# Optimization experiments

Measured on AMD Instinct MI355X. Metric: run time of the kernel, lower is better.

The kernel has to match this reference:

```python
import jax, jax.numpy as jnp
import numpy as np

IN_DIM = 256
OUT_DIM = 64   # per-head dim
NUM_HEADS = 8
B = 8
N = 1024


def setup_inputs() -> dict:
    key = jax.random.key(0)
    k_adj, k_h, kq, kk, kv, kbq, kbk, kbv = jax.random.split(key, 8)
    adj_matrix = jax.random.randint(k_adj, (N, N), 0, 2, dtype=jnp.int32)
    h = jax.random.normal(k_h, (B, N, IN_DIM), dtype=jnp.float32)
    s = 1.0 / np.sqrt(IN_DIM)
    Wq = jax.random.normal(kq, (IN_DIM, OUT_DIM * NUM_HEADS), dtype=jnp.float32) * s
    Wk = jax.random.normal(kk, (IN_DIM, OUT_DIM * NUM_HEADS), dtype=jnp.float32) * s
    Wv = jax.random.normal(kv, (IN_DIM, OUT_DIM * NUM_HEADS), dtype=jnp.float32) * s
    bq = jax.random.normal(kbq, (OUT_DIM * NUM_HEADS,), dtype=jnp.float32) * 0.01
    bk = jax.random.normal(kbk, (OUT_DIM * NUM_HEADS,), dtype=jnp.float32) * 0.01
    bv = jax.random.normal(kbv, (OUT_DIM * NUM_HEADS,), dtype=jnp.float32) * 0.01
    return {"adj_matrix": adj_matrix, "h": h, "Wq": Wq, "bq": bq,
            "Wk": Wk, "bk": bk, "Wv": Wv, "bv": bv}


def reference(adj_matrix, h, Wq, bq, Wk, bk, Wv, bv):
    B_, N_, _ = h.shape
    H, D = NUM_HEADS, OUT_DIM
    Qh = (h @ Wq + bq).reshape(B_, N_, H, D)
    Kh = (h @ Wk + bk).reshape(B_, N_, H, D)
    Vh = (h @ Wv + bv).reshape(B_, N_, H, D)
    scores = jnp.einsum('bnhd,bmhd->bhnm', Qh, Kh) / jnp.sqrt(jnp.float32(D))
    # adjacency mask broadcast over batch and heads (neigh_attention=True)
    scores = jnp.where(adj_matrix[None, None, :, :] == 0, -jnp.inf, scores)
    attn = jax.nn.softmax(scores, axis=-1)
    out = jnp.einsum('bhnm,bmhd->bnhd', attn, Vh)
    return out.reshape(B_, N_, H * D)
```

## Files before the change

kernel.cpp:

```cpp
#include <hip/hip_runtime.h>
#include <hip/hip_bf16.h>
#include <math.h>

#define IN_DIM 256
#define HD     512
#define NHEADS 8
#define DH     64
#define NSEQ   1024
#define BATCH  8

#define QSCALE 0.18033688011112042f

typedef unsigned short u16;
typedef unsigned int   u32;
typedef short bf16x8 __attribute__((ext_vector_type(8)));
typedef float f32x4  __attribute__((ext_vector_type(4)));
typedef float f32x16 __attribute__((ext_vector_type(16)));
typedef unsigned int u32x2 __attribute__((ext_vector_type(2)));

#if __has_builtin(__builtin_amdgcn_exp2f)
#define EXP2(x) __builtin_amdgcn_exp2f(x)
#else
#define EXP2(x) __expf(0.69314718056f * (x))
#endif

static __device__ __forceinline__ u16 f2bf(float x) {
    u32 u = __builtin_bit_cast(u32, x);
    u += 0x7FFFu + ((u >> 16) & 1u);
    return (u16)(u >> 16);
}
static __device__ __forceinline__ u32 pk(u16 a, u16 b) {
    return (u32)a | ((u32)b << 16);
}
static __device__ __forceinline__ u32 cvtpk(float a, float b) {
    __hip_bfloat162 t = __float22bfloat162_rn(make_float2(a, b));
    u32 r; __builtin_memcpy(&r, &t, 4);
    return r;
}
static __device__ __forceinline__ f32x16 maskinit(uint4 a, uint4 b) {
    f32x16 c;
    u32 ws[8] = {a.x, a.y, a.z, a.w, b.x, b.y, b.z, b.w};
#pragma unroll
    for (int i = 0; i < 8; ++i) {
        c[2 * i]     = __builtin_bit_cast(float, ws[i] << 16);
        c[2 * i + 1] = __builtin_bit_cast(float, ws[i] & 0xFFFF0000u);
    }
    return c;
}

static __device__ __forceinline__ void pswap(u32 &a, u32 &b) {
#if __has_builtin(__builtin_amdgcn_permlane32_swap)
    u32x2 r = __builtin_amdgcn_permlane32_swap(a, b, false, false);
    a = r.x; b = r.y;
#else
    const bool hi = (threadIdx.x & 32) != 0;
    u32 as = (u32)__shfl_xor((int)a, 32, 64);
    u32 bs = (u32)__shfl_xor((int)b, 32, 64);
    u32 na = hi ? bs : a;
    u32 nb = hi ? b  : as;
    a = na; b = nb;
#endif
}

#define MFMA32(a, b, c) __builtin_amdgcn_mfma_f32_32x32x16_bf16(a, b, c, 0, 0, 0)

#define GLOAD16(G, L)                                                          \
    __builtin_amdgcn_global_load_lds(                                          \
        (const __attribute__((address_space(1))) unsigned int*)(const void*)(G),\
        (__attribute__((address_space(3))) unsigned int*)(void*)(L), 16, 0, 0)

static __device__ __forceinline__ float sm_pack_half(const f32x16 st, bf16x8* pb) {
    float p[16];
#pragma unroll
    for (int r = 0; r < 16; ++r) p[r] = EXP2(st[r]);
    float t = (((p[0] + p[1]) + (p[2] + p[3])) + ((p[4] + p[5]) + (p[6] + p[7])))
            + (((p[8] + p[9]) + (p[10] + p[11])) + ((p[12] + p[13]) + (p[14] + p[15])));
    uint4 w0, w1;
    w0.x = cvtpk(p[0], p[1]);   w0.y = cvtpk(p[2], p[3]);
    w0.z = cvtpk(p[4], p[5]);   w0.w = cvtpk(p[6], p[7]);
    w1.x = cvtpk(p[8], p[9]);   w1.y = cvtpk(p[10], p[11]);
    w1.z = cvtpk(p[12], p[13]); w1.w = cvtpk(p[14], p[15]);
    pswap(w0.x, w1.x); pswap(w0.y, w1.y); pswap(w0.z, w1.z); pswap(w0.w, w1.w);
    pb[0] = __builtin_bit_cast(bf16x8, w0);
    pb[1] = __builtin_bit_cast(bf16x8, w1);
    return t;
}

__global__ __launch_bounds__(256)
void wtrans_kernel(const float* __restrict__ Wq, const float* __restrict__ Wk,
                   const float* __restrict__ Wv, const float* __restrict__ h,
                   u16* __restrict__ Wt, u16* __restrict__ hb)
{
    __shared__ float tile[64 * 65];
    const int bid = blockIdx.x, tid = threadIdx.x;

    if (bid >= 96) {
        const int ab = bid - 96;
        const float4* hs = (const float4*)h;
        uint2* hd = (uint2*)hb;
        const int base = ab * 4096 + tid;
#pragma unroll
        for (int j = 0; j < 16; ++j) {
            float4 v = hs[base + j * 256];
            uint2 o;
            o.x = cvtpk(v.x, v.y);
            o.y = cvtpk(v.z, v.w);
            hd[base + j * 256] = o;
        }
        return;
    }

    const int k0 = (bid & 3) * 64, n0 = ((bid >> 2) & 7) * 64, wsel = bid >> 5;
    const float* W = (wsel == 0) ? Wq : (wsel == 1) ? Wk : Wv;
    u16* Out = Wt + (size_t)wsel * HD * IN_DIM;

    const int r = tid >> 2, c0 = (tid & 3) * 16;
#pragma unroll
    for (int j = 0; j < 16; j += 4) {
        float4 v = *(const float4*)(W + (size_t)(k0 + r) * HD + n0 + c0 + j);
        tile[r * 65 + c0 + j + 0] = v.x; tile[r * 65 + c0 + j + 1] = v.y;
        tile[r * 65 + c0 + j + 2] = v.z; tile[r * 65 + c0 + j + 3] = v.w;
    }
    __syncthreads();
    const int n = tid >> 2, ks = (tid & 3) * 16;
    u16 o[16];
#pragma unroll
    for (int j = 0; j < 16; ++j) o[j] = f2bf(tile[(ks + j) * 65 + n]);
    uint4 u0, u1;
    u0.x = pk(o[0], o[1]);   u0.y = pk(o[2], o[3]);
    u0.z = pk(o[4], o[5]);   u0.w = pk(o[6], o[7]);
    u1.x = pk(o[8], o[9]);   u1.y = pk(o[10], o[11]);
    u1.z = pk(o[12], o[13]); u1.w = pk(o[14], o[15]);
    u16* dst = Out + (size_t)(n0 + n) * IN_DIM + k0 + ks;
    *(uint4*)(dst) = u0;
    *(uint4*)(dst + 8) = u1;
}

__global__ __launch_bounds__(256, 2)
void gemm_mask_kernel(const u16* __restrict__ hb, const u16* __restrict__ Wt,
                      const int* __restrict__ adj,
                      const float* __restrict__ bq, const float* __restrict__ bk,
                      const float* __restrict__ bv,
                      u16* __restrict__ Qg, u16* __restrict__ Kg,
                      u16* __restrict__ Vtg, u16* __restrict__ Madd3)
{
    __shared__ __align__(16) u16 lds[32768];
    const int tid = threadIdx.x;

    if (blockIdx.y >= 8) {
        int* tile = (int*)lds;
        const int abid = (blockIdx.y - 8) * 128 + blockIdx.x;
        const int tR = abid >> 4, tC = abid & 15;
        const int r = tid >> 2, cg = (tid & 3) * 16;
        const int* src = adj + (size_t)(tR * 64 + r) * NSEQ + tC * 64 + cg;
#pragma unroll
        for (int j = 0; j < 16; j += 4) {
            int4 a = *(const int4*)(src + j);
            tile[r * 65 + cg + j + 0] = a.x; tile[r * 65 + cg + j + 1] = a.y;
            tile[r * 65 + cg + j + 2] = a.z; tile[r * 65 + cg + j + 3] = a.w;
        }
        __syncthreads();
        const int q = tid >> 2, g4 = tid & 3, p0 = g4 * 16;
        u16 o[16];
#pragma unroll
        for (int j = 0; j < 16; ++j) {
            const int p = p0 + j;
            const int c = 32 * (p >> 5) + (p & 3) + 4 * ((p >> 4) & 1) + 8 * ((p >> 2) & 3);
            o[j] = (tile[q * 65 + c] == 0) ? (u16)0xFF7F : (u16)0;
        }
        uint4 u0, u1;
        u0.x = pk(o[0], o[1]);   u0.y = pk(o[2], o[3]);
        u0.z = pk(o[4], o[5]);   u0.w = pk(o[6], o[7]);
        u1.x = pk(o[8], o[9]);   u1.y = pk(o[10], o[11]);
        u1.z = pk(o[12], o[13]); u1.w = pk(o[14], o[15]);
        u16* dst = Madd3 + ((size_t)(tC * 4 + g4) * 1024 + tR * 64 + q) * 16;
        *(uint4*)(dst) = u0;
        *(uint4*)(dst + 8) = u1;
        return;
    }

    const int m0 = blockIdx.x * 64;
    const int hh = blockIdx.y;
    const int n0 = hh * 64;

    const int w = tid >> 6, lane = tid & 63;
    const int l31 = lane & 31, half = lane >> 5;
    const int mh = w & 1, nh = w >> 1;
    const int s7 = l31 & 7;

    const int lrow = lane >> 3, lgran = (lane & 7) ^ lrow;
    const int r0 = w * 16;
    const u16* ag = hb + (size_t)(m0 + r0 + lrow) * IN_DIM + lgran * 8;
    const u16* bg = Wt + (size_t)(n0 + r0 + lrow) * IN_DIM + lgran * 8;

#define STAGE_G(BUF, KK)                                                        \
    do {                                                                        \
        u16* a0 = lds + (BUF) * 4096 + r0 * 64;                                 \
        u16* b0 = lds + 8192 + (BUF) * 12288 + r0 * 64;                         \
        GLOAD16(ag + (KK) * 64,                                    a0);         \
        GLOAD16(ag + (KK) * 64 + 8 * IN_DIM,                       a0 + 512);   \
        GLOAD16(bg + (KK) * 64,                                    b0);         \
        GLOAD16(bg + (KK) * 64 + 8 * IN_DIM,                       b0 + 512);   \
        GLOAD16(bg + (KK) * 64 + (size_t)HD * IN_DIM,              b0 + 4096);  \
        GLOAD16(bg + (KK) * 64 + (size_t)HD * IN_DIM + 8 * IN_DIM, b0 + 4608);  \
        GLOAD16(bg + (KK) * 64 + (size_t)2 * HD * IN_DIM,          b0 + 8192);  \
        GLOAD16(bg + (KK) * 64 + (size_t)2 * HD * IN_DIM + 8 * IN_DIM, b0 + 8704); \
    } while (0)

    f32x16 acc[3] = {};
    const int arow = (32 * mh + l31) * 64;
    const int brow = (32 * nh + l31) * 64;

    STAGE_G(0, 0);
#pragma unroll
    for (int kk = 0; kk < 4; ++kk) {
        const int cur = kk & 1;
        __syncthreads();
        if (kk < 3) STAGE_G(1 - cur, kk + 1);
        const u16* Ac = lds + cur * 4096;
        const u16* Bc = lds + 8192 + cur * 12288;
#pragma unroll
        for (int s = 0; s < 4; ++s) {
            const int g = ((s * 2 + half) ^ s7) * 8;
            bf16x8 a = *(const bf16x8*)&Ac[arow + g];
#pragma unroll
            for (int wh = 0; wh < 3; ++wh) {
                bf16x8 b = *(const bf16x8*)&Bc[wh * 4096 + brow + g];
                acc[wh] = __builtin_amdgcn_mfma_f32_32x32x16_bf16(a, b, acc[wh], 0, 0, 0);
            }
        }
    }
#undef STAGE_G

    for (int which = 0; which < 2; ++which) {
        u16* T = lds;
        const float* bias = (which == 0) ? bq : bk;
        u16* Out = (which == 0) ? Qg : Kg;
        const float scale = (which == 0) ? QSCALE : 1.0f;
        const float bvv = bias[n0 + 32 * nh + l31];
        __syncthreads();
#pragma unroll
        for (int r = 0; r < 16; ++r) {
            const int row = 32 * mh + 4 * half + (r & 3) + 8 * (r >> 2);
            T[row * 72 + 32 * nh + l31] = f2bf((acc[which][r] + bvv) * scale);
        }
        __syncthreads();
        const int row = tid >> 2, qc = (tid & 3) * 16;
        u16* dst = Out + (size_t)(m0 + row) * HD + n0 + qc;
        const u16* srcT = &T[row * 72 + qc];
        *(uint4*)(dst)     = *(const uint4*)(srcT);
        *(uint4*)(dst + 8) = *(const uint4*)(srcT + 8);
    }

    {
        u16* T = lds;
        const int d = 32 * nh + l31;
        const float bvv = bv[n0 + d];
        __syncthreads();
#pragma unroll
        for (int g = 0; g < 4; ++g) {
            ushort4 o;
            o.x = f2bf(acc[2][4 * g + 0] + bvv);
            o.y = f2bf(acc[2][4 * g + 1] + bvv);
            o.z = f2bf(acc[2][4 * g + 2] + bvv);
            o.w = f2bf(acc[2][4 * g + 3] + bvv);
            *(ushort4*)&T[d * 72 + 32 * mh + 16 * half + 4 * g] = o;
        }
        __syncthreads();
        const int b = m0 >> 10, nloc = m0 & 1023;
        const int dd = tid >> 2, c = (tid & 3) * 16;
        u16* dst = Vtg + ((size_t)(b * NHEADS + hh) * DH + dd) * NSEQ + nloc + c;
        *(uint4*)(dst)     = *(uint4*)&T[dd * 72 + c];
        *(uint4*)(dst + 8) = *(uint4*)&T[dd * 72 + c + 8];
    }
}

__global__ __launch_bounds__(512, 4)
void attn_kernel(const u16* __restrict__ Madd3, const u16* __restrict__ Qg,
                 const u16* __restrict__ Kg, const u16* __restrict__ Vtg,
                 float* __restrict__ out)
{
    __shared__ __align__(16) u16 Ks[2][2][4096];
    __shared__ __align__(16) u16 Vs[2][2][4096];

    const int tid = threadIdx.x;
    const int w = tid >> 6, lane = tid & 63;
    const int team = w >> 2, j = w & 3;
    const int l31 = lane & 31, half = lane >> 5;
    const int bh = blockIdx.x, qt = blockIdx.y;
    const int b = bh >> 3;
    const int n0 = qt * 128;
    const size_t rowbase = (size_t)b * NSEQ;
    const int colbase = (bh & 7) * DH;
    const int q7 = l31 & 7;
    const int qA = j * 32 + l31;
    const int cbase = team * 8;

    const u16* qga = Qg + (rowbase + n0 + qA) * HD + colbase;
    bf16x8 qb[4];
#pragma unroll
    for (int s = 0; s < 4; ++s)
        qb[s] = *(const bf16x8*)(qga + s * 16 + half * 8);

    const int lrow = lane >> 3, lgran = (lane & 7) ^ lrow;
    const int br0 = j * 16, br1 = j * 16 + 8;
    const u16* kg0 = Kg + (rowbase + cbase * 64 + br0 + lrow) * HD + colbase + lgran * 8;
    const u16* kg1 = kg0 + (size_t)8 * HD;
    const u16* vg0 = Vtg + ((size_t)bh * DH + br0 + lrow) * NSEQ + cbase * 64 + lgran * 8;
    const u16* vg1 = vg0 + (size_t)8 * NSEQ;

#define STAGE(BUF, CH)                                                   \
    do {                                                                 \
        GLOAD16(kg0 + (size_t)(CH) * 64 * HD, &Ks[team][BUF][br0 * 64]); \
        GLOAD16(kg1 + (size_t)(CH) * 64 * HD, &Ks[team][BUF][br1 * 64]); \
        GLOAD16(vg0 + (CH) * 64,              &Vs[team][BUF][br0 * 64]); \
        GLOAD16(vg1 + (CH) * 64,              &Vs[team][BUF][br1 * 64]); \
    } while (0)

    const u16* mrow0 = Madd3 + (size_t)(cbase * 4 + half) * 16384 + (size_t)(n0 + qA) * 16;
    const u16* mrow1 = mrow0 + 32768;

    STAGE(0, 0);
    uint4 m0a = *(const uint4*)(mrow0);
    uint4 m0b = *(const uint4*)(mrow0 + 8);
    uint4 m1a = *(const uint4*)(mrow1);
    uint4 m1b = *(const uint4*)(mrow1 + 8);
    __syncthreads();

    float l = 0.f;
    f32x16 O0 = {}, O1 = {};

    for (int ch = 0; ch < 8; ++ch) {
        const int cur = ch & 1;
        const u16* Kc = &Ks[team][cur][0];
        const u16* Vc = &Vs[team][cur][0];

        if (ch < 7) STAGE(1 - cur, ch + 1);

        f32x16 s0 = maskinit(m0a, m0b);
        __builtin_amdgcn_s_setprio(1);
#pragma unroll
        for (int s = 0; s < 4; ++s) {
            const int g = ((s * 2 + half) ^ q7) * 8;
            bf16x8 ka = *(const bf16x8*)&Kc[l31 * 64 + g];
            s0 = MFMA32(ka, qb[s], s0);
        }
        __builtin_amdgcn_s_setprio(0);
        bf16x8 pb[2];
        l += sm_pack_half(s0, pb);

        __builtin_amdgcn_s_setprio(1);
#pragma unroll
        for (int s = 0; s < 2; ++s) {
            const int g = ((s * 2 + half) ^ q7) * 8;
            bf16x8 va0 = *(const bf16x8*)&Vc[l31 * 64 + g];
            bf16x8 va1 = *(const bf16x8*)&Vc[(32 + l31) * 64 + g];
            O0 = MFMA32(va0, pb[s], O0);
            O1 = MFMA32(va1, pb[s], O1);
        }
        __builtin_amdgcn_s_setprio(0);

        f32x16 s1 = maskinit(m1a, m1b);
        if (ch < 7) {
            const u16* mn0 = mrow0 + (size_t)(ch + 1) * 65536;
            const u16* mn1 = mrow1 + (size_t)(ch + 1) * 65536;
            m0a = *(const uint4*)(mn0);  m0b = *(const uint4*)(mn0 + 8);
            m1a = *(const uint4*)(mn1);  m1b = *(const uint4*)(mn1 + 8);
        }
        __builtin_amdgcn_s_setprio(1);
#pragma unroll
        for (int s = 0; s < 4; ++s) {
            const int g = ((s * 2 + half) ^ q7) * 8;
            bf16x8 ka = *(const bf16x8*)&Kc[(32 + l31) * 64 + g];
            s1 = MFMA32(ka, qb[s], s1);
        }
        __builtin_amdgcn_s_setprio(0);
        l += sm_pack_half(s1, pb);

        __builtin_amdgcn_s_setprio(1);
#pragma unroll
        for (int s = 2; s < 4; ++s) {
            const int g = ((s * 2 + half) ^ q7) * 8;
            bf16x8 va0 = *(const bf16x8*)&Vc[l31 * 64 + g];
            bf16x8 va1 = *(const bf16x8*)&Vc[(32 + l31) * 64 + g];
            O0 = MFMA32(va0, pb[s - 2], O0);
            O1 = MFMA32(va1, pb[s - 2], O1);
        }
        __builtin_amdgcn_s_setprio(0);
        __syncthreads();
    }
#undef STAGE

    float4* Oex = (float4*)&Ks[0][0][0];
    float*  Lex = (float*)&Vs[0][0][0];

    if (team == 1) {
#pragma unroll
        for (int g = 0; g < 4; ++g) {
            float4 t;
            t.x = O0[4 * g + 0]; t.y = O0[4 * g + 1];
            t.z = O0[4 * g + 2]; t.w = O0[4 * g + 3];
            Oex[(j * 8 + g) * 64 + lane] = t;
            t.x = O1[4 * g + 0]; t.y = O1[4 * g + 1];
            t.z = O1[4 * g + 2]; t.w = O1[4 * g + 3];
            Oex[(j * 8 + 4 + g) * 64 + lane] = t;
        }
        Lex[j * 64 + lane] = l;
    }
    __syncthreads();
    if (team == 0) {
        l += Lex[j * 64 + lane];
#pragma unroll
        for (int g = 0; g < 4; ++g) {
            float4 t0 = Oex[(j * 8 + g) * 64 + lane];
            float4 t1 = Oex[(j * 8 + 4 + g) * 64 + lane];
            O0[4 * g + 0] += t0.x; O0[4 * g + 1] += t0.y;
            O0[4 * g + 2] += t0.z; O0[4 * g + 3] += t0.w;
            O1[4 * g + 0] += t1.x; O1[4 * g + 1] += t1.y;
            O1[4 * g + 2] += t1.z; O1[4 * g + 3] += t1.w;
        }

        l += __shfl_xor(l, 32, 64);
        const float inv = 1.0f / l;

        float* orow = out + (rowbase + n0 + qA) * HD + colbase;
#pragma unroll
        for (int g = 0; g < 4; ++g) {
            const int d0 = 4 * half + 8 * g;
            float4 a0, a1;
            a0.x = O0[4 * g + 0] * inv; a0.y = O0[4 * g + 1] * inv;
            a0.z = O0[4 * g + 2] * inv; a0.w = O0[4 * g + 3] * inv;
            a1.x = O1[4 * g + 0] * inv; a1.y = O1[4 * g + 1] * inv;
            a1.z = O1[4 * g + 2] * inv; a1.w = O1[4 * g + 3] * inv;
            *(float4*)(orow + d0)      = a0;
            *(float4*)(orow + 32 + d0) = a1;
        }
    }
}

extern "C" void kernel_launch(void* const* d_in, const int* in_sizes, int n_in,
                              void* d_out, int out_size, void* d_ws, size_t ws_size,
                              hipStream_t stream) {
    const int*   adj = (const int*)d_in[0];
    const float* h   = (const float*)d_in[1];
    const float* Wq  = (const float*)d_in[2];
    const float* bq  = (const float*)d_in[3];
    const float* Wk  = (const float*)d_in[4];
    const float* bk  = (const float*)d_in[5];
    const float* Wv  = (const float*)d_in[6];
    const float* bv  = (const float*)d_in[7];
    float* outp = (float*)d_out;

    u16* Wt    = (u16*)d_ws;
    u16* Qg    = Wt + (size_t)3 * HD * IN_DIM;
    u16* Kg    = Qg + (size_t)BATCH * NSEQ * HD;
    u16* Vtg   = Kg + (size_t)BATCH * NSEQ * HD;
    u16* Madd3 = Vtg + (size_t)BATCH * NSEQ * HD;
    u16* hb    = Madd3 + (size_t)NSEQ * NSEQ;
    (void)ws_size;

    wtrans_kernel<<<224, 256, 0, stream>>>(Wq, Wk, Wv, h, Wt, hb);
    gemm_mask_kernel<<<dim3(BATCH * NSEQ / 64, 10), 256, 0, stream>>>(
        hb, Wt, adj, bq, bk, bv, Qg, Kg, Vtg, Madd3);
    attn_kernel<<<dim3(BATCH * NHEADS, NSEQ / 128, 2), 512, 0, stream>>>(
        Madd3, Qg, Kg, Vtg, outp);
}
```

Before: 150.8 us.

## Stage K/V through registers into padded LDS and drop duplicate grid z-dimension

```diff
diff --git a/kernel.cpp b/kernel.cpp
--- a/kernel.cpp
+++ b/kernel.cpp
@@ -68,6 +68,21 @@
     __builtin_amdgcn_global_load_lds(                                          \
         (const __attribute__((address_space(1))) unsigned int*)(const void*)(G),\
         (__attribute__((address_space(3))) unsigned int*)(void*)(L), 16, 0, 0)
+
+static __device__ __forceinline__ bf16x8 ldfrag(const u16* p) {
+    uint2 lo, hi;
+    __builtin_memcpy(&lo, p, 8);
+    __builtin_memcpy(&hi, p + 4, 8);
+    uint4 u;
+    u.x = lo.x; u.y = lo.y; u.z = hi.x; u.w = hi.y;
+    return __builtin_bit_cast(bf16x8, u);
+}
+static __device__ __forceinline__ void st16(u16* p, uint4 v) {
+    uint2 a, b;
+    a.x = v.x; a.y = v.y; b.x = v.z; b.y = v.w;
+    __builtin_memcpy(p, &a, 8);
+    __builtin_memcpy(p + 4, &b, 8);
+}
 
 static __device__ __forceinline__ float sm_pack_half(const f32x16 st, bf16x8* pb) {
     float p[16];
@@ -280,8 +295,7 @@
                  const u16* __restrict__ Kg, const u16* __restrict__ Vtg,
                  float* __restrict__ out)
 {
-    __shared__ __align__(16) u16 Ks[2][2][4096];
-    __shared__ __align__(16) u16 Vs[2][2][4096];
+    __shared__ __align__(16) u16 KV[2][2][2][4224];
 
     const int tid = threadIdx.x;
     const int w = tid >> 6, lane = tid & 63;
@@ -292,7 +306,6 @@
     const int n0 = qt * 128;
     const size_t rowbase = (size_t)b * NSEQ;
     const int colbase = (bh & 7) * DH;
-    const int q7 = l31 & 7;
     const int qA = j * 32 + l31;
     const int cbase = team * 8;
 
@@ -302,25 +315,35 @@
     for (int s = 0; s < 4; ++s)
         qb[s] = *(const bf16x8*)(qga + s * 16 + half * 8);
 
-    const int lrow = lane >> 3, lgran = (lane & 7) ^ lrow;
-    const int br0 = j * 16, br1 = j * 16 + 8;
-    const u16* kg0 = Kg + (rowbase + cbase * 64 + br0 + lrow) * HD + colbase + lgran * 8;
-    const u16* kg1 = kg0 + (size_t)8 * HD;
-    const u16* vg0 = Vtg + ((size_t)bh * DH + br0 + lrow) * NSEQ + cbase * 64 + lgran * 8;
-    const u16* vg1 = vg0 + (size_t)8 * NSEQ;
-
-#define STAGE(BUF, CH)                                                   \
-    do {                                                                 \
-        GLOAD16(kg0 + (size_t)(CH) * 64 * HD, &Ks[team][BUF][br0 * 64]); \
-        GLOAD16(kg1 + (size_t)(CH) * 64 * HD, &Ks[team][BUF][br1 * 64]); \
-        GLOAD16(vg0 + (CH) * 64,              &Vs[team][BUF][br0 * 64]); \
-        GLOAD16(vg1 + (CH) * 64,              &Vs[team][BUF][br1 * 64]); \
+    const int ttid = tid & 255;
+    const int srow = ttid >> 3, sg = ttid & 7;
+    const u16* kst = Kg + (rowbase + cbase * 64 + srow) * HD + colbase + sg * 8;
+    const u16* vst = Vtg + ((size_t)bh * DH + srow) * NSEQ + cbase * 64 + sg * 8;
+    const int wi0 = srow * 66 + sg * 8;
+    const int wi1 = (srow + 32) * 66 + sg * 8;
+
+    uint4 kr0, kr1, vr0, vr1;
+#define LOADR(CH)                                                         \
+    do {                                                                  \
+        kr0 = *(const uint4*)(kst + (size_t)(CH) * 64 * HD);              \
+        kr1 = *(const uint4*)(kst + (size_t)(CH) * 64 * HD + 32 * HD);    \
+        vr0 = *(const uint4*)(vst + (CH) * 64);                           \
+        vr1 = *(const uint4*)(vst + (CH) * 64 + 32 * NSEQ);               \
+    } while (0)
+#define WRITER(BUF)                                                       \
+    do {                                                                  \
+        u16* kd = &KV[team][BUF][0][0];                                   \
+        u16* vd = &KV[team][BUF][1][0];                                   \
+        st16(kd + wi0, kr0); st16(kd + wi1, kr1);                         \
+        st16(vd + wi0, vr0); st16(vd + wi1, vr1);                         \
     } while (0)
 
     const u16* mrow0 = Madd3 + (size_t)(cbase * 4 + half) * 16384 + (size_t)(n0 + qA) * 16;
     const u16* mrow1 = mrow0 + 32768;
 
-    STAGE(0, 0);
+    LOADR(0);
+    WRITER(0);
+    LOADR(1);
     uint4 m0a = *(const uint4*)(mrow0);
     uint4 m0b = *(const uint4*)(mrow0 + 8);
     uint4 m1a = *(const uint4*)(mrow1);
@@ -330,19 +353,22 @@
     float l = 0.f;
     f32x16 O0 = {}, O1 = {};
 
+    const int rb0 = l31 * 66, rb1 = (32 + l31) * 66;
+
     for (int ch = 0; ch < 8; ++ch) {
         const int cur = ch & 1;
-        const u16* Kc = &Ks[team][cur][0];
-        const u16* Vc = &Vs[team][cur][0];
-
-        if (ch < 7) STAGE(1 - cur, ch + 1);
+        const u16* Kc = &KV[team][cur][0][0];
+        const u16* Vc = &KV[team][cur][1][0];
+
+        if (ch < 7) WRITER(1 - cur);
+        if (ch < 6) LOADR(ch + 2);
 
         f32x16 s0 = maskinit(m0a, m0b);
         __builtin_amdgcn_s_setprio(1);
 #pragma unroll
         for (int s = 0; s < 4; ++s) {
-            const int g = ((s * 2 + half) ^ q7) * 8;
-            bf16x8 ka = *(const bf16x8*)&Kc[l31 * 64 + g];
+            const int g = (s * 2 + half) * 8;
+            bf16x8 ka = ldfrag(&Kc[rb0 + g]);
             s0 = MFMA32(ka, qb[s], s0);
         }
         __builtin_amdgcn_s_setprio(0);
@@ -352,9 +378,9 @@
         __builtin_amdgcn_s_setprio(1);
 #pragma unroll
         for (int s = 0; s < 2; ++s) {
-            const int g = ((s * 2 + half) ^ q7) * 8;
-            bf16x8 va0 = *(const bf16x8*)&Vc[l31 * 64 + g];
-            bf16x8 va1 = *(const bf16x8*)&Vc[(32 + l31) * 64 + g];
+            const int g = (s * 2 + half) * 8;
+            bf16x8 va0 = ldfrag(&Vc[rb0 + g]);
+            bf16x8 va1 = ldfrag(&Vc[rb1 + g]);
             O0 = MFMA32(va0, pb[s], O0);
             O1 = MFMA32(va1, pb[s], O1);
         }
@@ -370,8 +396,8 @@
         __builtin_amdgcn_s_setprio(1);
 #pragma unroll
         for (int s = 0; s < 4; ++s) {
-            const int g = ((s * 2 + half) ^ q7) * 8;
-            bf16x8 ka = *(const bf16x8*)&Kc[(32 + l31) * 64 + g];
+            const int g = (s * 2 + half) * 8;
+            bf16x8 ka = ldfrag(&Kc[rb1 + g]);
             s1 = MFMA32(ka, qb[s], s1);
         }
         __builtin_amdgcn_s_setprio(0);
@@ -380,19 +406,20 @@
         __builtin_amdgcn_s_setprio(1);
 #pragma unroll
         for (int s = 2; s < 4; ++s) {
-            const int g = ((s * 2 + half) ^ q7) * 8;
-            bf16x8 va0 = *(const bf16x8*)&Vc[l31 * 64 + g];
-            bf16x8 va1 = *(const bf16x8*)&Vc[(32 + l31) * 64 + g];
+            const int g = (s * 2 + half) * 8;
+            bf16x8 va0 = ldfrag(&Vc[rb0 + g]);
+            bf16x8 va1 = ldfrag(&Vc[rb1 + g]);
             O0 = MFMA32(va0, pb[s - 2], O0);
             O1 = MFMA32(va1, pb[s - 2], O1);
         }
         __builtin_amdgcn_s_setprio(0);
         __syncthreads();
     }
-#undef STAGE
-
-    float4* Oex = (float4*)&Ks[0][0][0];
-    float*  Lex = (float*)&Vs[0][0][0];
+#undef LOADR
+#undef WRITER
+
+    float4* Oex = (float4*)&KV[0][0][0][0];
+    float*  Lex = (float*)(&KV[0][0][0][0] + 16384);
 
     if (team == 1) {
 #pragma unroll
@@ -462,6 +489,6 @@
     wtrans_kernel<<<224, 256, 0, stream>>>(Wq, Wk, Wv, h, Wt, hb);
     gemm_mask_kernel<<<dim3(BATCH * NSEQ / 64, 10), 256, 0, stream>>>(
         hb, Wt, adj, bq, bk, bv, Qg, Kg, Vtg, Madd3);
-    attn_kernel<<<dim3(BATCH * NHEADS, NSEQ / 128, 2), 512, 0, stream>>>(
+    attn_kernel<<<dim3(BATCH * NHEADS, NSEQ / 128), 512, 0, stream>>>(
         Madd3, Qg, Kg, Vtg, outp);
 }
```

After: 154.2 us. 1.02x slower.
